# Optimization experiments

Measured on AMD Instinct MI355X. Metric: run time of the kernel, lower is better.

Reference implementation:

```python
import jax, jax.numpy as jnp
import numpy as np

B, N, C, H = 2, 2048, 256, 16
D = C // H  # head_dim = 16


def _res_linear(x, W, b):
    # ResidualMLP with num_layers=-1 and in_dim==out_dim, input/output residual: x + Linear(x)
    return x + x @ W.T + b


def _split_heads(z):
    # [B, N, H*D] -> [B, H, N, D]
    return z.reshape(B, N, H, D).transpose(0, 2, 1, 3)


def setup_inputs() -> dict:
    key = jax.random.key(0)
    ks = jax.random.split(key, 10)
    def lin(k):
        return 0.02 * jax.random.normal(k, (C, C), dtype=jnp.float32)
    inp = {
        'x': jax.random.normal(ks[0], (B, N, C), dtype=jnp.float32),
        'attention_mask': jnp.ones((B, N), dtype=jnp.float32),
        'Wq1': lin(ks[1]), 'bq1': jnp.zeros((C,), jnp.float32),
        'Wq2': lin(ks[2]), 'bq2': jnp.zeros((C,), jnp.float32),
        'Wq3': lin(ks[3]), 'bq3': jnp.zeros((C,), jnp.float32),
        'Wk1': lin(ks[4]), 'bk1': jnp.zeros((C,), jnp.float32),
        'Wk2': lin(ks[5]), 'bk2': jnp.zeros((C,), jnp.float32),
        'Wk3': lin(ks[6]), 'bk3': jnp.zeros((C,), jnp.float32),
        'Wv': lin(ks[7]), 'bv': jnp.zeros((C,), jnp.float32),
        'Wo': lin(ks[8]), 'bo': jnp.zeros((C,), jnp.float32),
        'gamma': jnp.ones((C,), jnp.float32),
        'beta': jnp.zeros((C,), jnp.float32),
    }
    return inp


def reference(x, attention_mask, Wq1, bq1, Wq2, bq2, Wq3, bq3,
              Wk1, bk1, Wk2, bk2, Wk3, bk3, Wv, bv, Wo, bo, gamma, beta):
    # residual single-linear projections (ResidualMLP num_layers=-1)
    q1 = _split_heads(_res_linear(x, Wq1, bq1))
    q2 = _split_heads(_res_linear(x, Wq2, bq2))
    q3 = _split_heads(_res_linear(x, Wq3, bq3))
    k1 = _split_heads(_res_linear(x, Wk1, bk1))
    k2 = _split_heads(_res_linear(x, Wk2, bk2))
    k3 = _split_heads(_res_linear(x, Wk3, bk3))
    v = _split_heads(_res_linear(x, Wv, bv))
    # kernel = identity; norm_q = norm_k = False
    mask = attention_mask[:, None, :, None]  # [B,1,N,1]
    q1, q2, q3 = q1 * mask, q2 * mask, q3 * mask
    k1, k2, k3, v = k1 * mask, k2 * mask, k3 * mask, v * mask
    scale = jnp.asarray(N, jnp.float32) ** -0.25
    k1, k2, k3, v = k1 * scale, k2 * scale, k3 * scale, v * scale
    # rank-4 state: [B,H,D,D,D,D]
    state = jnp.einsum('bhni,bhnj,bhnk,bhnl->bhijkl', k1, v, k2, k3, optimize=True)
    # contract queries with state: [B,H,N,D]
    out = jnp.einsum('bhni,bhijkl,bhnk,bhnl->bhnj', q1, state, q2, q3, optimize=True)
    out = out.transpose(0, 2, 1, 3).reshape(B, N, C)  # merge heads
    # LayerNorm(channel_dim), eps=1e-5
    mu = jnp.mean(out, axis=-1, keepdims=True)
    var = jnp.mean(jnp.square(out - mu), axis=-1, keepdims=True)
    out = (out - mu) * jax.lax.rsqrt(var + 1e-5) * gamma + beta
    out = out @ Wo.T + bo
    return out
```

## Files before the change

kernel.cpp:

```cpp
#include <hip/hip_runtime.h>
#include <hip/hip_bf16.h>


typedef _Float16 f16;
typedef _Float16 f16x8 __attribute__((ext_vector_type(8)));
typedef _Float16 f16x4 __attribute__((ext_vector_type(4)));
typedef float    f32x16 __attribute__((ext_vector_type(16)));
typedef uint32_t u32x4 __attribute__((ext_vector_type(4)));

#define MFMA32(a, b, c) __builtin_amdgcn_mfma_f32_32x32x16_f16((a), (b), (c), 0, 0, 0)

constexpr size_t OFF_XH  = 0;
constexpr size_t OFF_WH  = 2097152;
constexpr size_t OFF_BSC = 3014656;
constexpr size_t OFF_GH  = 3021824;
constexpr size_t OFF_RSG = 3152896;
constexpr size_t OFF_B2  = 3153920;
constexpr size_t OFF_Y   = 3154944;
constexpr size_t OFF_OPP = 17835008;
constexpr size_t OFF_O1  = 26223616;

struct W7 { const float* W[7]; const float* b[7]; };

__device__ __forceinline__ int toff(int row, int oct) {
    return row * 128 + (((oct) ^ (row & 7)) << 4);
}
__device__ __forceinline__ f16x8 ldfrag(const f16* base, int row, int oct) {
    return *(const f16x8*)((const char*)base + toff(row, oct));
}
__device__ __forceinline__ void stfrag(f16* base, int row, int oct, f16x8 v) {
    *(f16x8*)((char*)base + toff(row, oct)) = v;
}
__device__ __forceinline__ int drow(int reg, int l) {
    return (reg & 3) + ((reg >> 2) << 3) + ((l >> 5) << 2);
}
__device__ __forceinline__ void zero16(f32x16& v) {
#pragma unroll
    for (int i = 0; i < 16; ++i) v[i] = 0.f;
}
__device__ __forceinline__ uint32_t pkrtz(float a, float b) {
    auto h = __builtin_amdgcn_cvt_pkrtz(a, b);
    return __builtin_bit_cast(uint32_t, h);
}
__device__ __forceinline__ void pswap(uint32_t& x, uint32_t& y) {
    asm volatile("v_permlane32_swap_b32 %0, %1" : "+v"(x), "+v"(y));
}

__global__ __launch_bounds__(256) void k_prep(const float* __restrict__ x, W7 p,
                                              float scale,
                                              const float* __restrict__ Wo,
                                              const float* __restrict__ bo,
                                              const float* __restrict__ gamma,
                                              const float* __restrict__ beta,
                                              char* ws) {
    const int bid = blockIdx.x;
    if (bid < 2824) {
        f16* xh  = (f16*)(ws + OFF_XH);
        f16* Wh  = (f16*)(ws + OFF_WH);
        float* bsc = (float*)(ws + OFF_BSC);
        int idx = bid * 256 + threadIdx.x;
        if (idx < 262144) {
            float4 v = ((const float4*)x)[idx];
            f16x4 o; o[0] = (f16)v.x; o[1] = (f16)v.y; o[2] = (f16)v.z; o[3] = (f16)v.w;
            *(f16x4*)(xh + (size_t)idx * 4) = o;
        } else if (idx < 262144 + 458752) {
            int r = idx - 262144;
            int t = r >> 16, cc = r & 65535, c = cc >> 8, k = cc & 255;
            float v = p.W[t][cc] + (c == k ? 1.f : 0.f);
            if (t >= 3) v *= scale;
            Wh[r] = (f16)v;
        } else if (idx < 262144 + 458752 + 1792) {
            int r = idx - 262144 - 458752;
            int t = r >> 8;
            bsc[r] = p.b[t][r & 255] * (t >= 3 ? scale : 1.f);
        }
    } else {
        f16* Gh = (f16*)(ws + OFF_GH);
        float* rsg = (float*)(ws + OFF_RSG);
        float* B2  = (float*)(ws + OFF_B2);
        int c2 = bid - 2824, c = threadIdx.x;
        float wv = Wo[c2 * 256 + c];
        float g = gamma[c] * wv;
        float bb = beta[c] * wv;
        Gh[c2 * 256 + c] = (f16)g;
        __shared__ float sg[4], sb[4];
#pragma unroll
        for (int off = 32; off > 0; off >>= 1) { g += __shfl_down(g, off); bb += __shfl_down(bb, off); }
        if ((c & 63) == 0) { sg[c >> 6] = g; sb[c >> 6] = bb; }
        __syncthreads();
        if (c == 0) {
            rsg[c2] = sg[0] + sg[1] + sg[2] + sg[3];
            B2[c2]  = sb[0] + sb[1] + sb[2] + sb[3] + bo[c2];
        }
    }
}

__global__ __launch_bounds__(512) void k_lin7(const float* __restrict__ mask, char* ws) {
    const f16* xh = (const f16*)(ws + OFF_XH);
    const f16* Wh = (const f16*)(ws + OFF_WH);
    const float* bsc = (const float*)(ws + OFF_BSC);
    f16* Y = (f16*)(ws + OFF_Y);

    const int ct = blockIdx.x;
    const int rt = blockIdx.y;
    const int t = ct >> 1, half = ct & 1;
    const int tid = threadIdx.x, l = tid & 63, w = tid >> 6;
    const int wr = w >> 1, wc = w & 1;

    __shared__ f16 Xl[128 * 64];
    __shared__ f16 Wl[128 * 64];

    f32x16 acc[2];
    zero16(acc[0]); zero16(acc[1]);

    const f16* Wt = Wh + (size_t)t * 65536;
    for (int kt = 0; kt < 4; ++kt) {
        __syncthreads();
#pragma unroll
        for (int e = 0; e < 2; ++e) {
            int g = tid + 512 * e;
            int row = g >> 3, oct = g & 7;
            f16x8 vx = *(const f16x8*)(xh + (size_t)(rt * 128 + row) * 256 + kt * 64 + oct * 8);
            stfrag(Xl, row, oct, vx);
            f16x8 vw = *(const f16x8*)(Wt + (size_t)(half * 128 + row) * 256 + kt * 64 + oct * 8);
            stfrag(Wl, row, oct, vw);
        }
        __syncthreads();
#pragma unroll
        for (int s = 0; s < 4; ++s) {
            int g = s * 2 + (l >> 5);
            f16x8 a0 = ldfrag(Xl, wr * 32 + (l & 31), g);
            f16x8 b0 = ldfrag(Wl, wc * 64 + (l & 31), g);
            f16x8 b1 = ldfrag(Wl, wc * 64 + 32 + (l & 31), g);
            acc[0] = MFMA32(a0, b0, acc[0]);
            acc[1] = MFMA32(a0, b1, acc[1]);
        }
    }

#pragma unroll
    for (int mc = 0; mc < 2; ++mc)
#pragma unroll
        for (int reg = 0; reg < 16; ++reg) {
            int n = rt * 128 + wr * 32 + drow(reg, l);
            int c = half * 128 + wc * 64 + mc * 32 + (l & 31);
            float v = (acc[mc][reg] + bsc[t * 256 + c]) * mask[n];
            Y[(size_t)t * 1048576 + (size_t)n * 256 + c] = (f16)v;
        }
}

__global__ __launch_bounds__(256) void k_attn(char* ws) {
    const f16* Y = (const f16*)(ws + OFF_Y);
    float* OPP = (float*)(ws + OFF_OPP);

    const int nt = blockIdx.x;
    const int bh = blockIdx.y;
    const int ms = blockIdx.z;
    const int b = bh >> 4, hb = (bh & 15) * 16;
    const int tid = threadIdx.x, l = tid & 63, w = tid >> 6;
    const int lane31 = l & 31, lhi = l >> 5;
    const int n0 = nt * 256 + w * 64;

    __shared__ f16 kbuf[2][6144];
    __shared__ f16 btb[2][2048];

    f16x8 qf[3][2];
#pragma unroll
    for (int t = 0; t < 3; ++t)
#pragma unroll
        for (int nn = 0; nn < 2; ++nn)
            qf[t][nn] = *(const f16x8*)(Y + (size_t)t * 1048576 +
                        ((size_t)(b * 2048 + n0 + nn * 32 + lane31)) * 256 + hb + lhi * 8);

    f32x16 acc[2];
    zero16(acc[0]); zero16(acc[1]);
    f32x16 zzz; zero16(zzz);

    const int klane = lhi * 1024 + lane31 * 8;
    const int jj = lane31 & 15;
    int bvo[4][2];
#pragma unroll
    for (int sub = 0; sub < 4; ++sub)
#pragma unroll
        for (int h = 0; h < 2; ++h) {
            int g = sub * 4 + h * 2 + lhi;
            bvo[sub][h] = jj * 128 + (((g ^ (jj & 7)) << 3));
        }

    const int km = tid & 127, kdh = tid >> 7;
    const int vm = tid >> 1, vdh = tid & 1;
    const size_t mrow0 = (size_t)(b * 2048 + ms * 1024);
    const f16* Yk0 = Y + (size_t)3 * 1048576 + (mrow0 + km) * 256 + hb + kdh * 8;
    const f16* Yk1 = Yk0 + 1048576;
    const f16* Yk2 = Yk1 + 1048576;
    const f16* Yv  = Y + (size_t)6 * 1048576 + (mrow0 + vm) * 256 + hb + vdh * 8;
    const int kdst = kdh * 1024 + km * 8;

    f16x8 kp0, kp1, kp2, vp;
    kp0 = *(const f16x8*)(Yk0);
    kp1 = *(const f16x8*)(Yk1);
    kp2 = *(const f16x8*)(Yk2);
    vp  = *(const f16x8*)(Yv);
    {
        f16* kb = kbuf[0]; f16* bt = btb[0];
        *(f16x8*)(kb + kdst)        = kp0;
        *(f16x8*)(kb + 2048 + kdst) = kp1;
        *(f16x8*)(kb + 4096 + kdst) = kp2;
#pragma unroll
        for (int e = 0; e < 8; ++e) {
            int j = vdh * 8 + e;
            bt[j * 128 + (((vm >> 3) ^ e) << 3) + (vm & 7)] = vp[e];
        }
    }

    int cur = 0;
    for (int c = 0; c < 8; ++c) {
        __syncthreads();
        if (c < 7) {
            size_t adv = (size_t)(c + 1) * 128 * 256;
            kp0 = *(const f16x8*)(Yk0 + adv);
            kp1 = *(const f16x8*)(Yk1 + adv);
            kp2 = *(const f16x8*)(Yk2 + adv);
            vp  = *(const f16x8*)(Yv + adv);
        }
        const f16* kb = kbuf[cur];
        const f16* bt = btb[cur];
#pragma unroll
        for (int sub = 0; sub < 4; ++sub) {
            f16x8 kf0 = *(const f16x8*)(kb + klane + sub * 256);
            f16x8 kf1 = *(const f16x8*)(kb + klane + 2048 + sub * 256);
            f16x8 kf2 = *(const f16x8*)(kb + klane + 4096 + sub * 256);
            f16x8 bv1 = *(const f16x8*)(bt + bvo[sub][0]);
            f16x8 bv2 = *(const f16x8*)(bt + bvo[sub][1]);
#pragma unroll
            for (int nn = 0; nn < 2; ++nn) {
                f32x16 D1 = MFMA32(kf0, qf[0][nn], zzz);
                f32x16 D2 = MFMA32(kf1, qf[1][nn], zzz);
                f32x16 D3 = MFMA32(kf2, qf[2][nn], zzz);
#pragma unroll
                for (int i = 0; i < 16; ++i) D1[i] *= D2[i];
#pragma unroll
                for (int i = 0; i < 16; ++i) D1[i] *= D3[i];
                uint32_t p01 = pkrtz(D1[0], D1[1]),   p23 = pkrtz(D1[2], D1[3]);
                uint32_t p45 = pkrtz(D1[4], D1[5]),   p67 = pkrtz(D1[6], D1[7]);
                uint32_t p89 = pkrtz(D1[8], D1[9]),   pAB = pkrtz(D1[10], D1[11]);
                uint32_t pCD = pkrtz(D1[12], D1[13]), pEF = pkrtz(D1[14], D1[15]);
                pswap(p01, p45);
                pswap(p23, p67);
                pswap(p89, pCD);
                pswap(pAB, pEF);
                u32x4 A1 = {p01, p23, p45, p67};
                u32x4 A2 = {p89, pAB, pCD, pEF};
                acc[nn] = MFMA32(__builtin_bit_cast(f16x8, A1), bv1, acc[nn]);
                acc[nn] = MFMA32(__builtin_bit_cast(f16x8, A2), bv2, acc[nn]);
            }
        }
        if (c < 7) {
            f16* kb2 = kbuf[cur ^ 1]; f16* bt2 = btb[cur ^ 1];
            *(f16x8*)(kb2 + kdst)        = kp0;
            *(f16x8*)(kb2 + 2048 + kdst) = kp1;
            *(f16x8*)(kb2 + 4096 + kdst) = kp2;
#pragma unroll
            for (int e = 0; e < 8; ++e) {
                int j = vdh * 8 + e;
                bt2[j * 128 + (((vm >> 3) ^ e) << 3) + (vm & 7)] = vp[e];
            }
        }
        cur ^= 1;
    }

    if (lane31 < 16) {
        float* outp = OPP + (size_t)ms * 1048576;
#pragma unroll
        for (int nn = 0; nn < 2; ++nn)
#pragma unroll
            for (int reg = 0; reg < 16; ++reg) {
                int n = n0 + nn * 32 + drow(reg, l);
                outp[((size_t)(b * 2048) + n) * 256 + hb + lane31] = acc[nn][reg];
            }
    }
}

__global__ __launch_bounds__(256) void k_osum(char* ws) {
    const float* P0 = (const float*)(ws + OFF_OPP);
    const float* P1 = P0 + 1048576;
    f16* O1 = (f16*)(ws + OFF_O1);
    int i = (blockIdx.x * 256 + threadIdx.x) * 8;
    float4 a0 = *(const float4*)(P0 + i), a1 = *(const float4*)(P0 + i + 4);
    float4 b0 = *(const float4*)(P1 + i), b1 = *(const float4*)(P1 + i + 4);
    f16x8 o;
    o[0] = (f16)(a0.x + b0.x); o[1] = (f16)(a0.y + b0.y);
    o[2] = (f16)(a0.z + b0.z); o[3] = (f16)(a0.w + b0.w);
    o[4] = (f16)(a1.x + b1.x); o[5] = (f16)(a1.y + b1.y);
    o[6] = (f16)(a1.z + b1.z); o[7] = (f16)(a1.w + b1.w);
    *(f16x8*)(O1 + i) = o;
}

__global__ __launch_bounds__(256) void k_final(float* __restrict__ out, char* ws) {
    const f16* O1 = (const f16*)(ws + OFF_O1);
    const f16* Gh = (const f16*)(ws + OFF_GH);
    const float* rsg = (const float*)(ws + OFF_RSG);
    const float* B2 = (const float*)(ws + OFF_B2);

    const int ct = blockIdx.x;
    const int rt = blockIdx.y;
    const int tid = threadIdx.x, l = tid & 63, w = tid >> 6;
    const int wr = w >> 1, wc = w & 1;

    __shared__ f16 Xl[128 * 64];
    __shared__ f16 Wl[128 * 64];
    __shared__ float muL[128], rsL[128];

    float sum[4] = {0.f, 0.f, 0.f, 0.f}, sumsq[4] = {0.f, 0.f, 0.f, 0.f};

    f32x16 acc[2][2];
#pragma unroll
    for (int m = 0; m < 2; ++m)
#pragma unroll
        for (int mc = 0; mc < 2; ++mc) zero16(acc[m][mc]);

    for (int kt = 0; kt < 4; ++kt) {
        __syncthreads();
#pragma unroll
        for (int e = 0; e < 4; ++e) {
            int g = tid + 256 * e;
            int row = g >> 3, oct = g & 7;
            f16x8 vx = *(const f16x8*)(O1 + (size_t)(rt * 128 + row) * 256 + kt * 64 + oct * 8);
            stfrag(Xl, row, oct, vx);
#pragma unroll
            for (int q = 0; q < 8; ++q) { float f = (float)vx[q]; sum[e] += f; sumsq[e] += f * f; }
            f16x8 vw = *(const f16x8*)(Gh + (size_t)(ct * 128 + row) * 256 + kt * 64 + oct * 8);
            stfrag(Wl, row, oct, vw);
        }
        __syncthreads();
#pragma unroll
        for (int s = 0; s < 4; ++s) {
            int g = s * 2 + (l >> 5);
            f16x8 a0 = ldfrag(Xl, wr * 64 + (l & 31), g);
            f16x8 a1 = ldfrag(Xl, wr * 64 + 32 + (l & 31), g);
            f16x8 b0 = ldfrag(Wl, wc * 64 + (l & 31), g);
            f16x8 b1 = ldfrag(Wl, wc * 64 + 32 + (l & 31), g);
            acc[0][0] = MFMA32(a0, b0, acc[0][0]);
            acc[0][1] = MFMA32(a0, b1, acc[0][1]);
            acc[1][0] = MFMA32(a1, b0, acc[1][0]);
            acc[1][1] = MFMA32(a1, b1, acc[1][1]);
        }
    }

#pragma unroll
    for (int e = 0; e < 4; ++e) {
#pragma unroll
        for (int off = 1; off < 8; off <<= 1) {
            sum[e] += __shfl_xor(sum[e], off);
            sumsq[e] += __shfl_xor(sumsq[e], off);
        }
    }
    if ((tid & 7) == 0) {
#pragma unroll
        for (int e = 0; e < 4; ++e) {
            int row = (tid >> 3) + 32 * e;
            float m = sum[e] * (1.f / 256.f);
            float var = sumsq[e] * (1.f / 256.f) - m * m;
            muL[row] = m;
            rsL[row] = rsqrtf(var + 1e-5f);
        }
    }
    __syncthreads();

#pragma unroll
    for (int m = 0; m < 2; ++m)
#pragma unroll
        for (int mc = 0; mc < 2; ++mc)
#pragma unroll
            for (int reg = 0; reg < 16; ++reg) {
                int nloc = wr * 64 + m * 32 + drow(reg, l);
                int n = rt * 128 + nloc;
                int c2 = ct * 128 + wc * 64 + mc * 32 + (l & 31);
                float v = rsL[nloc] * (acc[m][mc][reg] - muL[nloc] * rsg[c2]) + B2[c2];
                out[(size_t)n * 256 + c2] = v;
            }
}

extern "C" void kernel_launch(void* const* d_in, const int* in_sizes, int n_in,
                              void* d_out, int out_size, void* d_ws, size_t ws_size,
                              hipStream_t stream) {
    (void)in_sizes; (void)n_in; (void)out_size; (void)ws_size;
    const float* x    = (const float*)d_in[0];
    const float* mask = (const float*)d_in[1];
    W7 p;
    for (int t = 0; t < 7; ++t) {
        p.W[t] = (const float*)d_in[2 + 2 * t];
        p.b[t] = (const float*)d_in[3 + 2 * t];
    }
    const float* Wo    = (const float*)d_in[16];
    const float* bo    = (const float*)d_in[17];
    const float* gamma = (const float*)d_in[18];
    const float* beta  = (const float*)d_in[19];
    char* ws = (char*)d_ws;

    const float scale = 0.14865088937534013f;

    k_prep <<<3080, 256, 0, stream>>>(x, p, scale, Wo, bo, gamma, beta, ws);
    k_lin7 <<<dim3(14, 32), 512, 0, stream>>>(mask, ws);
    k_attn <<<dim3(8, 32, 2), 256, 0, stream>>>(ws);
    k_osum <<<512, 256, 0, stream>>>(ws);
    k_final<<<dim3(2, 32), 256, 0, stream>>>((float*)d_out, ws);
}
```

Baseline: 69.18 us.

## Fuse split-K partial sum into final GEMM and halve attention rows per block

The attention kernel now gives each wave 32 query rows instead of 64, doubling the grid to 1024 blocks, and adds an occupancy hint of 4 blocks per SIMD. Partial outputs are written as fp16 instead of fp32. The separate reduction kernel is removed, and the final LayerNorm+GEMM kernel sums the two split-K partials as it loads them. This cuts one launch and some memory traffic and should improve occupancy, at the cost of reloading the K/V tiles twice as often per query row and extra fp16 rounding on the partials.

```diff
diff --git a/kernel.cpp b/kernel.cpp
--- a/kernel.cpp
+++ b/kernel.cpp
@@ -18,7 +18,6 @@
 constexpr size_t OFF_B2  = 3153920;
 constexpr size_t OFF_Y   = 3154944;
 constexpr size_t OFF_OPP = 17835008;
-constexpr size_t OFF_O1  = 26223616;
 
 struct W7 { const float* W[7]; const float* b[7]; };
 
@@ -148,9 +147,9 @@
         }
 }
 
-__global__ __launch_bounds__(256) void k_attn(char* ws) {
+__global__ __launch_bounds__(256, 4) void k_attn(char* ws) {
     const f16* Y = (const f16*)(ws + OFF_Y);
-    float* OPP = (float*)(ws + OFF_OPP);
+    f16* OPP = (f16*)(ws + OFF_OPP);
 
     const int nt = blockIdx.x;
     const int bh = blockIdx.y;
@@ -158,33 +157,24 @@
     const int b = bh >> 4, hb = (bh & 15) * 16;
     const int tid = threadIdx.x, l = tid & 63, w = tid >> 6;
     const int lane31 = l & 31, lhi = l >> 5;
-    const int n0 = nt * 256 + w * 64;
+    const int n0 = nt * 128 + w * 32;
 
     __shared__ f16 kbuf[2][6144];
     __shared__ f16 btb[2][2048];
 
-    f16x8 qf[3][2];
-#pragma unroll
-    for (int t = 0; t < 3; ++t)
-#pragma unroll
-        for (int nn = 0; nn < 2; ++nn)
-            qf[t][nn] = *(const f16x8*)(Y + (size_t)t * 1048576 +
-                        ((size_t)(b * 2048 + n0 + nn * 32 + lane31)) * 256 + hb + lhi * 8);
-
-    f32x16 acc[2];
-    zero16(acc[0]); zero16(acc[1]);
+    f16x8 qf0, qf1, qf2;
+    {
+        size_t base = ((size_t)(b * 2048 + n0 + lane31)) * 256 + hb + lhi * 8;
+        qf0 = *(const f16x8*)(Y + base);
+        qf1 = *(const f16x8*)(Y + 1048576 + base);
+        qf2 = *(const f16x8*)(Y + 2097152 + base);
+    }
+
+    f32x16 acc; zero16(acc);
     f32x16 zzz; zero16(zzz);
 
     const int klane = lhi * 1024 + lane31 * 8;
     const int jj = lane31 & 15;
-    int bvo[4][2];
-#pragma unroll
-    for (int sub = 0; sub < 4; ++sub)
-#pragma unroll
-        for (int h = 0; h < 2; ++h) {
-            int g = sub * 4 + h * 2 + lhi;
-            bvo[sub][h] = jj * 128 + (((g ^ (jj & 7)) << 3));
-        }
 
     const int km = tid & 127, kdh = tid >> 7;
     const int vm = tid >> 1, vdh = tid & 1;
@@ -229,30 +219,27 @@
             f16x8 kf0 = *(const f16x8*)(kb + klane + sub * 256);
             f16x8 kf1 = *(const f16x8*)(kb + klane + 2048 + sub * 256);
             f16x8 kf2 = *(const f16x8*)(kb + klane + 4096 + sub * 256);
-            f16x8 bv1 = *(const f16x8*)(bt + bvo[sub][0]);
-            f16x8 bv2 = *(const f16x8*)(bt + bvo[sub][1]);
-#pragma unroll
-            for (int nn = 0; nn < 2; ++nn) {
-                f32x16 D1 = MFMA32(kf0, qf[0][nn], zzz);
-                f32x16 D2 = MFMA32(kf1, qf[1][nn], zzz);
-                f32x16 D3 = MFMA32(kf2, qf[2][nn], zzz);
-#pragma unroll
-                for (int i = 0; i < 16; ++i) D1[i] *= D2[i];
-#pragma unroll
-                for (int i = 0; i < 16; ++i) D1[i] *= D3[i];
-                uint32_t p01 = pkrtz(D1[0], D1[1]),   p23 = pkrtz(D1[2], D1[3]);
-                uint32_t p45 = pkrtz(D1[4], D1[5]),   p67 = pkrtz(D1[6], D1[7]);
-                uint32_t p89 = pkrtz(D1[8], D1[9]),   pAB = pkrtz(D1[10], D1[11]);
-                uint32_t pCD = pkrtz(D1[12], D1[13]), pEF = pkrtz(D1[14], D1[15]);
-                pswap(p01, p45);
-                pswap(p23, p67);
-                pswap(p89, pCD);
-                pswap(pAB, pEF);
-                u32x4 A1 = {p01, p23, p45, p67};
-                u32x4 A2 = {p89, pAB, pCD, pEF};
-                acc[nn] = MFMA32(__builtin_bit_cast(f16x8, A1), bv1, acc[nn]);
-                acc[nn] = MFMA32(__builtin_bit_cast(f16x8, A2), bv2, acc[nn]);
-            }
+            f16x8 bv1 = *(const f16x8*)(bt + jj * 128 + (((sub * 4 + lhi) ^ (jj & 7)) << 3));
+            f16x8 bv2 = *(const f16x8*)(bt + jj * 128 + (((sub * 4 + 2 + lhi) ^ (jj & 7)) << 3));
+            f32x16 D = MFMA32(kf0, qf0, zzz);
+            f32x16 E = MFMA32(kf1, qf1, zzz);
+#pragma unroll
+            for (int i = 0; i < 16; ++i) D[i] *= E[i];
+            E = MFMA32(kf2, qf2, zzz);
+#pragma unroll
+            for (int i = 0; i < 16; ++i) D[i] *= E[i];
+            uint32_t p01 = pkrtz(D[0], D[1]),   p23 = pkrtz(D[2], D[3]);
+            uint32_t p45 = pkrtz(D[4], D[5]),   p67 = pkrtz(D[6], D[7]);
+            uint32_t p89 = pkrtz(D[8], D[9]),   pAB = pkrtz(D[10], D[11]);
+            uint32_t pCD = pkrtz(D[12], D[13]), pEF = pkrtz(D[14], D[15]);
+            pswap(p01, p45);
+            pswap(p23, p67);
+            pswap(p89, pCD);
+            pswap(pAB, pEF);
+            u32x4 A1 = {p01, p23, p45, p67};
+            u32x4 A2 = {p89, pAB, pCD, pEF};
+            acc = MFMA32(__builtin_bit_cast(f16x8, A1), bv1, acc);
+            acc = MFMA32(__builtin_bit_cast(f16x8, A2), bv2, acc);
         }
         if (c < 7) {
             f16* kb2 = kbuf[cur ^ 1]; f16* bt2 = btb[cur ^ 1];
@@ -269,34 +256,18 @@
     }
 
     if (lane31 < 16) {
-        float* outp = OPP + (size_t)ms * 1048576;
-#pragma unroll
-        for (int nn = 0; nn < 2; ++nn)
-#pragma unroll
-            for (int reg = 0; reg < 16; ++reg) {
-                int n = n0 + nn * 32 + drow(reg, l);
-                outp[((size_t)(b * 2048) + n) * 256 + hb + lane31] = acc[nn][reg];
-            }
-    }
-}
-
-__global__ __launch_bounds__(256) void k_osum(char* ws) {
-    const float* P0 = (const float*)(ws + OFF_OPP);
-    const float* P1 = P0 + 1048576;
-    f16* O1 = (f16*)(ws + OFF_O1);
-    int i = (blockIdx.x * 256 + threadIdx.x) * 8;
-    float4 a0 = *(const float4*)(P0 + i), a1 = *(const float4*)(P0 + i + 4);
-    float4 b0 = *(const float4*)(P1 + i), b1 = *(const float4*)(P1 + i + 4);
-    f16x8 o;
-    o[0] = (f16)(a0.x + b0.x); o[1] = (f16)(a0.y + b0.y);
-    o[2] = (f16)(a0.z + b0.z); o[3] = (f16)(a0.w + b0.w);
-    o[4] = (f16)(a1.x + b1.x); o[5] = (f16)(a1.y + b1.y);
-    o[6] = (f16)(a1.z + b1.z); o[7] = (f16)(a1.w + b1.w);
-    *(f16x8*)(O1 + i) = o;
+        f16* outp = OPP + (size_t)ms * 1048576;
+#pragma unroll
+        for (int reg = 0; reg < 16; ++reg) {
+            int n = n0 + drow(reg, l);
+            outp[((size_t)(b * 2048) + n) * 256 + hb + lane31] = (f16)acc[reg];
+        }
+    }
 }
 
 __global__ __launch_bounds__(256) void k_final(float* __restrict__ out, char* ws) {
-    const f16* O1 = (const f16*)(ws + OFF_O1);
+    const f16* P0 = (const f16*)(ws + OFF_OPP);
+    const f16* P1 = P0 + 1048576;
     const f16* Gh = (const f16*)(ws + OFF_GH);
     const float* rsg = (const float*)(ws + OFF_RSG);
     const float* B2 = (const float*)(ws + OFF_B2);
@@ -324,10 +295,17 @@
         for (int e = 0; e < 4; ++e) {
             int g = tid + 256 * e;
             int row = g >> 3, oct = g & 7;
-            f16x8 vx = *(const f16x8*)(O1 + (size_t)(rt * 128 + row) * 256 + kt * 64 + oct * 8);
+            size_t idx = (size_t)(rt * 128 + row) * 256 + kt * 64 + oct * 8;
+            f16x8 va = *(const f16x8*)(P0 + idx);
+            f16x8 vb = *(const f16x8*)(P1 + idx);
+            f16x8 vx;
+#pragma unroll
+            for (int q = 0; q < 8; ++q) {
+                float f = (float)va[q] + (float)vb[q];
+                vx[q] = (f16)f;
+                sum[e] += f; sumsq[e] += f * f;
+            }
             stfrag(Xl, row, oct, vx);
-#pragma unroll
-            for (int q = 0; q < 8; ++q) { float f = (float)vx[q]; sum[e] += f; sumsq[e] += f * f; }
             f16x8 vw = *(const f16x8*)(Gh + (size_t)(ct * 128 + row) * 256 + kt * 64 + oct * 8);
             stfrag(Wl, row, oct, vw);
         }
@@ -401,7 +379,6 @@
 
     k_prep <<<3080, 256, 0, stream>>>(x, p, scale, Wo, bo, gamma, beta, ws);
     k_lin7 <<<dim3(14, 32), 512, 0, stream>>>(mask, ws);
-    k_attn <<<dim3(8, 32, 2), 256, 0, stream>>>(ws);
-    k_osum <<<512, 256, 0, stream>>>(ws);
+    k_attn <<<dim3(16, 32, 2), 256, 0, stream>>>(ws);
     k_final<<<dim3(2, 32), 256, 0, stream>>>((float*)d_out, ws);
 }
```

Measured after the change: 69.29 us. Within noise of the previous version (+0.2%).
